# Optimization experiments

Hardware: AMD Instinct MI355X
Metric: run time of the kernel (lower is better)

Reference implementation:

```python
import jax, jax.numpy as jnp
import numpy as np

WIN_LEN = 3072
HOP = 192


def hann_window(n):
    # torch.hann_window(n, periodic=False)
    k = jnp.arange(n, dtype=jnp.float32)
    return 0.5 - 0.5 * jnp.cos(2.0 * jnp.pi * k / (n - 1))


def setup_inputs() -> dict:
    key = jax.random.key(0)
    k1, k2 = jax.random.split(key)
    B, C, F, T = 8, 1, 128, 1000
    filter_bands = jax.random.uniform(k1, (B, C, F, T), dtype=jnp.float32)
    # torch: rand*2-1 uniform in [-1, 1)
    noise = jax.random.uniform(k2, (B, C, (T - 1) * HOP), dtype=jnp.float32) * 2.0 - 1.0
    return {"filter_bands": filter_bands, "noise": noise}


def reference(filter_bands, noise):
    B, C, F, T = filter_bands.shape
    half = WIN_LEN // 2  # 1536
    padded = jnp.pad(noise, ((0, 0), (0, 0), (half, half)))
    L = padded.shape[-1]  # (T-1)*HOP + 2*half
    # unfold: [T, WIN_LEN] gather indices, frames [B, C, T, WIN_LEN]
    frame_idx = jnp.arange(T)[:, None] * HOP + jnp.arange(WIN_LEN)[None, :]
    frames = padded[:, :, frame_idx]
    # nearest interpolation of bands F -> half (torch 'nearest': floor(i*F/out))
    src = (jnp.arange(half) * F) // half
    filt = filter_bands[:, :, src, :]          # [B, C, half, T]
    filt = jnp.transpose(filt, (0, 1, 3, 2))   # [B, C, T, half]
    filt = jnp.pad(filt, ((0, 0), (0, 0), (0, 0), (1, 0)))  # prepend DC zero -> half+1 bins
    spec = jnp.fft.rfft(frames)                # [B, C, T, half+1] complex
    out_frames = jnp.fft.irfft(filt * spec, n=WIN_LEN)  # [B, C, T, WIN_LEN]
    out_frames = out_frames * hann_window(WIN_LEN)
    # overlap-add (F.fold with stride HOP)
    out = jnp.zeros((B, C, L), dtype=out_frames.dtype)
    out = out.at[:, :, frame_idx.reshape(-1)].add(out_frames.reshape(B, C, -1))
    return out[:, :, half:-half]
```

## Files before the change

### kernel.cpp

```cpp
#include <hip/hip_runtime.h>
#include <hip/hip_fp16.h>

#define NFFT 3072
#define THREADS 256
#define HOP 192
#define HALF 1536
#define TFRAMES 1000
#define OUTLEN 191808
#define NBANDS 128
#define PI_F 3.14159265358979323846f
#define SEGLEN 3264
#define NSEG 500

__device__ __forceinline__ float2 cadd(float2 a,float2 b){return make_float2(a.x+b.x,a.y+b.y);}
__device__ __forceinline__ float2 csub(float2 a,float2 b){return make_float2(a.x-b.x,a.y-b.y);}
__device__ __forceinline__ float2 cmul(float2 a,float2 b){
    return make_float2(fmaf(a.x,b.x,-a.y*b.y), fmaf(a.x,b.y,a.y*b.x));
}
__device__ __forceinline__ float2 cmuln_i(float2 a){return make_float2(a.y,-a.x);}
__device__ __forceinline__ float2 cneg(float2 a){return make_float2(-a.x,-a.y);}

__device__ __forceinline__ int IDX(int i){ return i + (i>>4); }

__device__ __forceinline__ void dft4(float2 a0,float2 a1,float2 a2,float2 a3,
                                     float2&y0,float2&y1,float2&y2,float2&y3){
    float2 e0=cadd(a0,a2), e1=csub(a0,a2), o0=cadd(a1,a3), o1=csub(a1,a3);
    y0=cadd(e0,o0); y2=csub(e0,o0);
    float2 io=make_float2(-o1.y,o1.x);
    y1=csub(e1,io); y3=cadd(e1,io);
}
__device__ __forceinline__ void dft3(float2 a0,float2 a1,float2 a2,
                                     float2&y0,float2&y1,float2&y2){
    float2 s=cadd(a1,a2), d=csub(a1,a2);
    y0=cadd(a0,s);
    float2 t=make_float2(a0.x-0.5f*s.x, a0.y-0.5f*s.y);
    const float S3=0.86602540378443864676f;
    float2 id=make_float2(S3*d.y,-S3*d.x);
    y1=cadd(t,id); y2=csub(t,id);
}

__device__ __forceinline__ void dft12(float2 a[12], float2 o[12]){
    float2 u[3][4];
    #pragma unroll
    for(int n2=0;n2<3;++n2)
        dft4(a[n2],a[3+n2],a[6+n2],a[9+n2],u[n2][0],u[n2][1],u[n2][2],u[n2][3]);
    const float2 W1=make_float2( 0.86602540378443865f,-0.5f);
    const float2 W2=make_float2( 0.5f,-0.86602540378443865f);
    const float2 W4=make_float2(-0.5f,-0.86602540378443865f);
    u[1][1]=cmul(u[1][1],W1); u[1][2]=cmul(u[1][2],W2); u[1][3]=cmuln_i(u[1][3]);
    u[2][1]=cmul(u[2][1],W2); u[2][2]=cmul(u[2][2],W4); u[2][3]=cneg(u[2][3]);
    #pragma unroll
    for(int k1=0;k1<4;++k1)
        dft3(u[0][k1],u[1][k1],u[2][k1], o[k1],o[k1+4],o[k1+8]);
}

__device__ __forceinline__ void dft16(float2 a[16], float2 o[16]){
    float2 u[4][4];
    #pragma unroll
    for(int n2=0;n2<4;++n2)
        dft4(a[n2],a[4+n2],a[8+n2],a[12+n2],u[n2][0],u[n2][1],u[n2][2],u[n2][3]);
    const float C16=0.92387953251128674f, S16=0.38268343236508977f, R2=0.70710678118654752f;
    const float2 W1=make_float2( C16,-S16), W2=make_float2( R2,-R2), W3=make_float2( S16,-C16);
    const float2 W6=make_float2(-R2,-R2),  W9=make_float2(-C16, S16);
    u[1][1]=cmul(u[1][1],W1); u[1][2]=cmul(u[1][2],W2);   u[1][3]=cmul(u[1][3],W3);
    u[2][1]=cmul(u[2][1],W2); u[2][2]=cmuln_i(u[2][2]);   u[2][3]=cmul(u[2][3],W6);
    u[3][1]=cmul(u[3][1],W3); u[3][2]=cmul(u[3][2],W6);   u[3][3]=cmul(u[3][3],W9);
    #pragma unroll
    for(int k1=0;k1<4;++k1)
        dft4(u[0][k1],u[1][k1],u[2][k1],u[3][k1], o[k1],o[k1+4],o[k1+8],o[k1+12]);
}

template<int R>
__device__ __forceinline__ void twiddle_pows(float2* o, float ang){
    float s,c; __sincosf(ang,&s,&c);
    float2 w1=make_float2(c,s);
    float2 w2=cmul(w1,w1);
    float2 w3=cmul(w2,w1);
    float2 w4=cmul(w2,w2);
    o[1]=cmul(o[1],w1); o[2]=cmul(o[2],w2); o[3]=cmul(o[3],w3);
    float2 w8=cmul(w4,w4);
    float2 w5=cmul(w4,w1), w6=cmul(w4,w2), w7=cmul(w4,w3);
    o[4]=cmul(o[4],w4); o[5]=cmul(o[5],w5); o[6]=cmul(o[6],w6); o[7]=cmul(o[7],w7);
    float2 w9=cmul(w8,w1), w10=cmul(w8,w2), w11=cmul(w8,w3);
    o[8]=cmul(o[8],w8); o[9]=cmul(o[9],w9); o[10]=cmul(o[10],w10); o[11]=cmul(o[11],w11);
    if constexpr (R>12){
        float2 w12=cmul(w8,w4), w13=cmul(w8,w5), w14=cmul(w8,w6), w15=cmul(w8,w7);
        o[12]=cmul(o[12],w12); o[13]=cmul(o[13],w13); o[14]=cmul(o[14],w14); o[15]=cmul(o[15],w15);
    }
}

__device__ __forceinline__ void stageB(float2* A, int tid){
    const bool act = tid < 192;
    float2 o[16];
    int q=0,p=0;
    if(act){
        q = tid % 12; p = tid / 12;
        float2 a[16];
        int ib = IDX(q + 12*p);
        #pragma unroll
        for(int l=0;l<16;++l) a[l] = A[ib + 204*l];
        dft16(a,o);
        twiddle_pows<16>(o, -2.0f*PI_F*(float)p*(1.0f/256.0f));
    }
    __syncthreads();
    if(act){
        #pragma unroll
        for(int j=0;j<16;++j) A[IDX(q + 192*p + 12*j)] = o[j];
    }
    __syncthreads();
}

template<bool USE_WS>
__global__ __launch_bounds__(THREADS,4)
void filtered_noise_kernel(const float* __restrict__ fb,
                           const float* __restrict__ noise,
                           __half* __restrict__ ws,
                           float* __restrict__ out)
{
    __shared__ float2 A[NFFT + NFFT/16];
    __shared__ float gf[2*NBANDS];

    const int tid = threadIdx.x;
    const int b   = blockIdx.x & 7;
    const int tp  = blockIdx.x >> 3;
    const int t0  = 2*tp;
    const float* nz = noise + (size_t)b * OUTLEN;
    const int base0 = t0*HOP - HALF;

    gf[tid] = fb[((size_t)b*NBANDS + (tid & 127))*TFRAMES + t0 + (tid >> 7)];

    {
        float2 a[12], o[12];
        #pragma unroll
        for(int l=0;l<12;++l){
            int i0 = base0 + tid + 256*l;
            float x0 = (i0 >= 0 && i0 < OUTLEN) ? nz[i0] : 0.0f;
            int i1 = i0 + HOP;
            float x1 = (i1 >= 0 && i1 < OUTLEN) ? nz[i1] : 0.0f;
            a[l] = make_float2(x0, x1);
        }
        dft12(a,o);
        twiddle_pows<12>(o, -2.0f*PI_F*(float)tid*(1.0f/3072.0f));
        #pragma unroll
        for(int j=0;j<12;++j) A[IDX(12*tid + j)] = o[j];
    }
    __syncthreads();

    stageB(A, tid);

    {
        const bool act = tid < 192;
        float2 o[16];
        if(act){
            float2 a[16];
            int ib = IDX(tid);
            #pragma unroll
            for(int l=0;l<16;++l) a[l] = A[ib + 204*l];
            dft16(a,o);
        }
        __syncthreads();
        if(act){
            int ib = IDX(tid);
            #pragma unroll
            for(int j=0;j<16;++j) A[ib + 204*j] = o[j];
        }
        __syncthreads();
    }

    {
        const int p = tid;
        float2 z[12], zm[12];
        {
            int ib = IDX(p);
            #pragma unroll
            for(int l=0;l<12;++l) z[l] = A[ib + 272*l];
        }
        {
            int pm = (p==0) ? 0 : (256 - p);
            int ib = IDX(pm);
            #pragma unroll
            for(int l=0;l<12;++l) zm[l] = A[ib + 272*l];
        }
        float2 w[12];
        #pragma unroll
        for(int l=0;l<12;++l){
            int k = p + 256*l;
            int j = (k <= HALF) ? k : (NFFT - k);
            float aa = 0.0f, bb = 0.0f;
            if(j){
                int band = (j-1)/12;
                float Gx = gf[band], Gy = gf[NBANDS + band];
                aa = 0.5f*(Gx+Gy); bb = 0.5f*(Gx-Gy);
            }
            float2 Zm = (p==0) ? ((l==0) ? z[0] : z[12-l]) : zm[11-l];
            w[l] = make_float2( fmaf(aa, z[l].x,  bb*Zm.x),
                                fmaf(-aa, z[l].y, bb*Zm.y) );
        }
        float2 o[12];
        dft12(w,o);
        twiddle_pows<12>(o, -2.0f*PI_F*(float)p*(1.0f/3072.0f));
        __syncthreads();
        #pragma unroll
        for(int j=0;j<12;++j) A[IDX(12*p + j)] = o[j];
        __syncthreads();
    }

    stageB(A, tid);

    {
        const bool act = tid < 192;
        if(act){
            float2 a[16], o[16];
            int ib = IDX(tid);
            #pragma unroll
            for(int l=0;l<16;++l) a[l] = A[ib + 204*l];
            dft16(a,o);
            const float invN = 1.0f/(float)NFFT;
            float prev_vy = 0.0f;
            __half* seg = USE_WS ? (ws + (size_t)(b*NSEG + tp)*SEGLEN) : nullptr;
            float* outb = USE_WS ? nullptr : (out + (size_t)b*OUTLEN);
            #pragma unroll
            for(int j=0;j<17;++j){
                int c = tid + 192*j;
                float val = prev_vy;
                if (j < 16){
                    float h = 0.5f - 0.5f*__cosf(2.0f*PI_F*(float)c*(1.0f/3071.0f));
                    float s = invN*h;
                    val    += o[j].x * s;
                    prev_vy = -o[j].y * s;
                }
                if (USE_WS){
                    seg[c] = __float2half(val);
                } else {
                    int p0 = base0 + c;
                    if (p0 >= 0 && p0 < OUTLEN) atomicAdd(&outb[p0], val);
                }
            }
        }
    }
}

__global__ __launch_bounds__(256)
void ola_reduce_kernel(const __half* __restrict__ ws, float* __restrict__ out)
{
    const int b = blockIdx.x & 7;
    const int n = (blockIdx.x >> 3)*256 + threadIdx.x;
    if (n >= OUTLEN) return;
    int tp1 = (n + 1536) / 384;            if (tp1 > NSEG-1) tp1 = NSEG-1;
    int tp0 = (n > 1727) ? (n - 1344) / 384 : 0;
    const __half* wb = ws + (size_t)b*NSEG*SEGLEN;
    float s = 0.0f;
    #pragma unroll
    for (int i = 0; i < 9; ++i){
        int tp = tp0 + i;
        if (tp <= tp1)
            s += __half2float(wb[tp*SEGLEN + (n + 1536 - 384*tp)]);
    }
    out[(size_t)b*OUTLEN + n] = s;
}

extern "C" void kernel_launch(void* const* d_in, const int* in_sizes, int n_in,
                              void* d_out, int out_size, void* d_ws, size_t ws_size,
                              hipStream_t stream)
{
    const float* fb    = (const float*)d_in[0];
    const float* noise = (const float*)d_in[1];
    float* out = (float*)d_out;

    const int B = in_sizes[1] / OUTLEN;
    const size_t need = (size_t)B * NSEG * SEGLEN * sizeof(__half);

    dim3 grid1(B * NSEG);

    if (ws_size >= need){
        filtered_noise_kernel<true><<<grid1, THREADS, 0, stream>>>(
            fb, noise, (__half*)d_ws, out);
        dim3 grid2(B * ((OUTLEN + 255)/256));
        ola_reduce_kernel<<<grid2, 256, 0, stream>>>((const __half*)d_ws, out);
    } else {
        hipMemsetAsync(out, 0, (size_t)out_size * sizeof(float), stream);
        filtered_noise_kernel<false><<<grid1, THREADS, 0, stream>>>(
            fb, noise, nullptr, out);
    }
}
```

Measured before the change: 158.0 us.

## Process four frames per block with shared-memory overlap-add accumulation

Each block now handles two frame pairs (four frames) in sequence and accumulates their overlapping windowed outputs in a shared-memory buffer before writing a single, longer fp16 segment. This halves the number of workspace segments and the number of reads per output sample in the reduction kernel, cutting global write and read traffic. The shared padding scheme also changes from one pad per 16 elements to one per 32. The costs are extra shared memory per block (the C buffer), fewer blocks in the grid, and serialized FFT work within each block, which may reduce occupancy and parallelism.

```diff
diff --git a/kernel.cpp b/kernel.cpp
--- a/kernel.cpp
+++ b/kernel.cpp
@@ -9,8 +9,9 @@
 #define OUTLEN 191808
 #define NBANDS 128
 #define PI_F 3.14159265358979323846f
-#define SEGLEN 3264
-#define NSEG 500
+#define SEGLEN 3648
+#define NSB 250
+#define SEGSTRIDE 768
 
 __device__ __forceinline__ float2 cadd(float2 a,float2 b){return make_float2(a.x+b.x,a.y+b.y);}
 __device__ __forceinline__ float2 csub(float2 a,float2 b){return make_float2(a.x-b.x,a.y-b.y);}
@@ -20,7 +21,7 @@
 __device__ __forceinline__ float2 cmuln_i(float2 a){return make_float2(a.y,-a.x);}
 __device__ __forceinline__ float2 cneg(float2 a){return make_float2(-a.x,-a.y);}
 
-__device__ __forceinline__ int IDX(int i){ return i + (i>>4); }
+__device__ __forceinline__ int IDXF(int i){ return i + (i>>5); }
 
 __device__ __forceinline__ void dft4(float2 a0,float2 a1,float2 a2,float2 a3,
                                      float2&y0,float2&y1,float2&y2,float2&y3){
@@ -89,45 +90,36 @@
     }
 }
 
-__device__ __forceinline__ void stageB(float2* A, int tid){
+__device__ __forceinline__ void stageB(float2* __restrict__ A, int tid){
     const bool act = tid < 192;
     float2 o[16];
     int q=0,p=0;
     if(act){
         q = tid % 12; p = tid / 12;
         float2 a[16];
-        int ib = IDX(q + 12*p);
-        #pragma unroll
-        for(int l=0;l<16;++l) a[l] = A[ib + 204*l];
+        int ib = IDXF(q + 12*p);
+        #pragma unroll
+        for(int l=0;l<16;++l) a[l] = A[ib + 198*l];
         dft16(a,o);
         twiddle_pows<16>(o, -2.0f*PI_F*(float)p*(1.0f/256.0f));
     }
     __syncthreads();
     if(act){
         #pragma unroll
-        for(int j=0;j<16;++j) A[IDX(q + 192*p + 12*j)] = o[j];
-    }
-    __syncthreads();
-}
-
-template<bool USE_WS>
-__global__ __launch_bounds__(THREADS,4)
-void filtered_noise_kernel(const float* __restrict__ fb,
-                           const float* __restrict__ noise,
-                           __half* __restrict__ ws,
-                           float* __restrict__ out)
+        for(int j=0;j<16;++j) A[IDXF(q + 192*p + 12*j)] = o[j];
+    }
+    __syncthreads();
+}
+
+__device__ __forceinline__ void process_pair(
+    const float* __restrict__ nz, const float* __restrict__ fbb,
+    float2* __restrict__ A, float* __restrict__ C, float* __restrict__ gf,
+    const int tid, const int t0, const int cb, const bool act)
 {
-    __shared__ float2 A[NFFT + NFFT/16];
-    __shared__ float gf[2*NBANDS];
-
-    const int tid = threadIdx.x;
-    const int b   = blockIdx.x & 7;
-    const int tp  = blockIdx.x >> 3;
-    const int t0  = 2*tp;
-    const float* nz = noise + (size_t)b * OUTLEN;
+    __syncthreads();
+    gf[tid] = fbb[(size_t)(tid & 127)*TFRAMES + t0 + (tid >> 7)];
+
     const int base0 = t0*HOP - HALF;
-
-    gf[tid] = fb[((size_t)b*NBANDS + (tid & 127))*TFRAMES + t0 + (tid >> 7)];
 
     {
         float2 a[12], o[12];
@@ -142,27 +134,26 @@
         dft12(a,o);
         twiddle_pows<12>(o, -2.0f*PI_F*(float)tid*(1.0f/3072.0f));
         #pragma unroll
-        for(int j=0;j<12;++j) A[IDX(12*tid + j)] = o[j];
+        for(int j=0;j<12;++j) A[IDXF(12*tid + j)] = o[j];
     }
     __syncthreads();
 
     stageB(A, tid);
 
     {
-        const bool act = tid < 192;
         float2 o[16];
         if(act){
             float2 a[16];
-            int ib = IDX(tid);
+            int ib = IDXF(tid);
             #pragma unroll
-            for(int l=0;l<16;++l) a[l] = A[ib + 204*l];
+            for(int l=0;l<16;++l) a[l] = A[ib + 198*l];
             dft16(a,o);
         }
         __syncthreads();
         if(act){
-            int ib = IDX(tid);
+            int ib = IDXF(tid);
             #pragma unroll
-            for(int j=0;j<16;++j) A[ib + 204*j] = o[j];
+            for(int j=0;j<16;++j) A[ib + 198*j] = o[j];
         }
         __syncthreads();
     }
@@ -171,15 +162,15 @@
         const int p = tid;
         float2 z[12], zm[12];
         {
-            int ib = IDX(p);
+            int ib = IDXF(p);
             #pragma unroll
-            for(int l=0;l<12;++l) z[l] = A[ib + 272*l];
+            for(int l=0;l<12;++l) z[l] = A[ib + 264*l];
         }
         {
             int pm = (p==0) ? 0 : (256 - p);
-            int ib = IDX(pm);
+            int ib = IDXF(pm);
             #pragma unroll
-            for(int l=0;l<12;++l) zm[l] = A[ib + 272*l];
+            for(int l=0;l<12;++l) zm[l] = A[ib + 264*l];
         }
         float2 w[12];
         #pragma unroll
@@ -201,40 +192,81 @@
         twiddle_pows<12>(o, -2.0f*PI_F*(float)p*(1.0f/3072.0f));
         __syncthreads();
         #pragma unroll
-        for(int j=0;j<12;++j) A[IDX(12*p + j)] = o[j];
+        for(int j=0;j<12;++j) A[IDXF(12*p + j)] = o[j];
         __syncthreads();
     }
 
     stageB(A, tid);
 
-    {
-        const bool act = tid < 192;
-        if(act){
-            float2 a[16], o[16];
-            int ib = IDX(tid);
-            #pragma unroll
-            for(int l=0;l<16;++l) a[l] = A[ib + 204*l];
-            dft16(a,o);
-            const float invN = 1.0f/(float)NFFT;
-            float prev_vy = 0.0f;
-            __half* seg = USE_WS ? (ws + (size_t)(b*NSEG + tp)*SEGLEN) : nullptr;
-            float* outb = USE_WS ? nullptr : (out + (size_t)b*OUTLEN);
-            #pragma unroll
-            for(int j=0;j<17;++j){
-                int c = tid + 192*j;
-                float val = prev_vy;
-                if (j < 16){
-                    float h = 0.5f - 0.5f*__cosf(2.0f*PI_F*(float)c*(1.0f/3071.0f));
-                    float s = invN*h;
-                    val    += o[j].x * s;
-                    prev_vy = -o[j].y * s;
-                }
-                if (USE_WS){
-                    seg[c] = __float2half(val);
-                } else {
-                    int p0 = base0 + c;
-                    if (p0 >= 0 && p0 < OUTLEN) atomicAdd(&outb[p0], val);
-                }
+    if(act){
+        float2 a[16], o[16];
+        int ib = IDXF(tid);
+        #pragma unroll
+        for(int l=0;l<16;++l) a[l] = A[ib + 198*l];
+        dft16(a,o);
+        const float invN = 1.0f/(float)NFFT;
+        float prev_vy = 0.0f;
+        #pragma unroll
+        for(int j=0;j<17;++j){
+            float val = prev_vy;
+            if (j < 16){
+                int n = tid + 192*j;
+                float h = 0.5f - 0.5f*__cosf(2.0f*PI_F*(float)n*(1.0f/3071.0f));
+                float s = invN*h;
+                val    += o[j].x * s;
+                prev_vy = -o[j].y * s;
+            }
+            C[cb + tid + 192*j] += val;
+        }
+    }
+}
+
+template<bool USE_WS>
+__global__ __launch_bounds__(THREADS,4)
+void filtered_noise_kernel(const float* __restrict__ fb,
+                           const float* __restrict__ noise,
+                           __half* __restrict__ ws,
+                           float* __restrict__ out)
+{
+    __shared__ float2 A[NFFT + NFFT/32];
+    __shared__ float  C[SEGLEN];
+    __shared__ float  gf[2*NBANDS];
+
+    const int tid = threadIdx.x;
+    const int b    = blockIdx.x & 7;
+    const int sseg = blockIdx.x >> 3;
+    const int T0   = 4*sseg;
+    const float* nz  = noise + (size_t)b * OUTLEN;
+    const float* fbb = fb + (size_t)b * NBANDS * TFRAMES;
+    const int blockbase = T0*HOP - HALF;
+    const bool act = tid < 192;
+
+    #pragma unroll
+    for(int i=0;i<15;++i){
+        int c = tid + 256*i;
+        if (c < SEGLEN) C[c] = 0.0f;
+    }
+
+    process_pair(nz, fbb, A, C, gf, tid, T0,     0,   act);
+    process_pair(nz, fbb, A, C, gf, tid, T0 + 2, 384, act);
+
+    __syncthreads();
+
+    if (USE_WS){
+        __half* seg = ws + (size_t)(b*NSB + sseg)*SEGLEN;
+        #pragma unroll
+        for(int i=0;i<15;++i){
+            int c = tid + 256*i;
+            if (c < SEGLEN) seg[c] = __float2half(C[c]);
+        }
+    } else {
+        float* outb = out + (size_t)b * OUTLEN;
+        #pragma unroll
+        for(int i=0;i<15;++i){
+            int c = tid + 256*i;
+            if (c < SEGLEN){
+                int p = blockbase + c;
+                if (p >= 0 && p < OUTLEN) atomicAdd(&outb[p], C[c]);
             }
         }
     }
@@ -246,15 +278,15 @@
     const int b = blockIdx.x & 7;
     const int n = (blockIdx.x >> 3)*256 + threadIdx.x;
     if (n >= OUTLEN) return;
-    int tp1 = (n + 1536) / 384;            if (tp1 > NSEG-1) tp1 = NSEG-1;
-    int tp0 = (n > 1727) ? (n - 1344) / 384 : 0;
-    const __half* wb = ws + (size_t)b*NSEG*SEGLEN;
+    int tp1 = (n + HALF) / SEGSTRIDE;      if (tp1 > NSB-1) tp1 = NSB-1;
+    int tp0 = (n > 2111) ? (n - 1344) / SEGSTRIDE : 0;
+    const __half* wb = ws + (size_t)b*NSB*SEGLEN;
     float s = 0.0f;
     #pragma unroll
-    for (int i = 0; i < 9; ++i){
+    for (int i = 0; i < 5; ++i){
         int tp = tp0 + i;
         if (tp <= tp1)
-            s += __half2float(wb[tp*SEGLEN + (n + 1536 - 384*tp)]);
+            s += __half2float(wb[tp*SEGLEN + (n + HALF - SEGSTRIDE*tp)]);
     }
     out[(size_t)b*OUTLEN + n] = s;
 }
@@ -268,9 +300,9 @@
     float* out = (float*)d_out;
 
     const int B = in_sizes[1] / OUTLEN;
-    const size_t need = (size_t)B * NSEG * SEGLEN * sizeof(__half);
-
-    dim3 grid1(B * NSEG);
+    const size_t need = (size_t)B * NSB * SEGLEN * sizeof(__half);
+
+    dim3 grid1(B * NSB);
 
     if (ws_size >= need){
         filtered_noise_kernel<true><<<grid1, THREADS, 0, stream>>>(
```

After: 176.3 us. +11.6%, slower.
